# Kernel tuning notes

Measured on AMD Instinct MI355X. Metric: run time of the kernel, lower is better.

The kernel has to match this reference:

```python
import jax, jax.numpy as jnp
import numpy as np

H = 2048
NBINS = 256

def setup_inputs() -> dict:
    key = jax.random.key(0)
    k1, k2, k3, k4 = jax.random.split(key, 4)
    input_data = jax.random.uniform(k1, (1, 3, H, H), jnp.float32, -1.0, 1.0)
    target_data = jax.random.uniform(k2, (1, 3, H, H), jnp.float32, -1.0, 1.0)
    mask_src = (jax.random.uniform(k3, (1, 1, H, H)) > 0.5).astype(jnp.float32)
    mask_tar = (jax.random.uniform(k4, (1, 1, H, H)) > 0.5).astype(jnp.float32)
    return {"input_data": input_data, "target_data": target_data,
            "mask_src": mask_src, "mask_tar": mask_tar}


def _de_norm(x):
    # (x+1)/2 clamped to [0,1]
    return jnp.clip((x + 1.0) * 0.5, 0.0, 1.0)


def _masked_cdf(img, mask):
    # img: [3,H,W] in [0,255]; mask: [H,W] 0/1 weights.
    # Equivalent to np.histogram(masked_pixels, bins=256, range=(0,255)) per
    # channel followed by normalized cumsum: weighted bincount over all pixels.
    bins = jnp.clip(jnp.floor(img * (NBINS / 255.0)).astype(jnp.int32), 0, NBINS - 1)
    offs = bins + (jnp.arange(3, dtype=jnp.int32) * NBINS)[:, None, None]
    w = jnp.broadcast_to(mask, img.shape).reshape(-1)
    hist = jax.ops.segment_sum(w, offs.reshape(-1), num_segments=3 * NBINS)
    hist = hist.reshape(3, NBINS)
    cdf = jnp.cumsum(hist, axis=1)
    total = jnp.maximum(cdf[:, -1:], 1.0)  # number of masked pixels
    return cdf / total


def _cal_trans(dst_cdf, ref_cdf):
    # Faithful vectorization of PSGAN cal_trans: for i in 1..255, table[i] is
    # the first j in 1..255 with ref_cdf[j-1] <= dst_cdf[i] <= ref_cdf[j],
    # else i; table[0]=0, table[255]=255.
    j0 = jnp.searchsorted(ref_cdf, dst_cdf, side='left')
    cand = jnp.clip(j0, 1, NBINS - 1)
    ok = (ref_cdf[cand - 1] <= dst_cdf) & (ref_cdf[cand] >= dst_cdf)
    idx = jnp.arange(NBINS)
    table = jnp.where(ok, cand, idx)
    table = table.at[0].set(0).at[NBINS - 1].set(NBINS - 1)
    return table


def _histogram_loss(input_data, target_data, mask_src, mask_tar):
    inp = _de_norm(input_data)[0] * 255.0   # [3,H,W]
    tar = _de_norm(target_data)[0] * 255.0  # [3,H,W]
    ms = mask_src[0, 0]  # [H,W]
    mt = mask_tar[0, 0]
    input_masked = inp * ms
    target_masked = tar * mt

    cdf_dst = _masked_cdf(input_masked, ms)   # [3,256]
    cdf_ref = _masked_cdf(target_masked, mt)  # [3,256]
    tables = jax.vmap(_cal_trans)(cdf_dst, cdf_ref)  # [3,256] int

    # remap masked pixels through per-channel LUT (int() truncation)
    pix = jnp.clip(input_masked.astype(jnp.int32), 0, NBINS - 1)  # [3,H,W]
    matched = jnp.take_along_axis(tables, pix.reshape(3, -1), axis=1)
    matched = matched.reshape(input_masked.shape).astype(input_masked.dtype)
    input_match = jnp.where(ms[None] != 0, matched, input_masked)
    input_match = jax.lax.stop_gradient(input_match)  # to_var(requires_grad=False)

    return jnp.mean(jnp.abs(input_masked - input_match))


def reference(input_data, target_data, mask_src, mask_tar):
    return _histogram_loss(input_data, target_data, mask_src, mask_tar)
```

## Files before the change

kernel.cpp:

```cpp
#include <hip/hip_runtime.h>

#define HH 2048
#define NPIX (HH * HH)
#define NBINS 256
#define NQ (NPIX / 4)

#define GHIST_WORDS (6 * NBINS)
#define GPK_WORDS   (3 * NBINS)
#define WS_ZERO_BYTES (GHIST_WORDS * 4 + GPK_WORDS * 8)

#define FRAC_BITS 22
#define CNT_SHIFT 42
#define FRAC_MASK ((1ULL << CNT_SHIFT) - 1)

__device__ __forceinline__ float denorm255(float x) {
    return fminf(fmaxf((x + 1.0f) * 0.5f, 0.0f), 1.0f) * 255.0f;
}

__global__ __launch_bounds__(512, 8) void fused_hist(
        const float* __restrict__ in, const float* __restrict__ tar,
        const float* __restrict__ ms, const float* __restrict__ mt,
        unsigned* __restrict__ ghist, unsigned long long* __restrict__ gpk) {
    __shared__ unsigned lhs[3 * NBINS];
    __shared__ unsigned lht[3 * NBINS];
    __shared__ unsigned long long lpk[3 * NBINS];
    for (int i = threadIdx.x; i < 3 * NBINS; i += blockDim.x) {
        lhs[i] = 0u; lht[i] = 0u; lpk[i] = 0ull;
    }
    __syncthreads();

    const float BSCALE = 256.0f / 255.0f;
    const float FSCALE = 4194304.0f;
    const int stride = gridDim.x * blockDim.x;
    for (int idx = blockIdx.x * blockDim.x + threadIdx.x; idx < NQ; idx += stride) {
        float4 m4 = ((const float4*)ms)[idx];
        float4 t4 = ((const float4*)mt)[idx];
        float mv[4] = {m4.x, m4.y, m4.z, m4.w};
        float tv[4] = {t4.x, t4.y, t4.z, t4.w};
        #pragma unroll
        for (int ch = 0; ch < 3; ++ch) {
            float4 a = ((const float4*)(in  + (size_t)ch * NPIX))[idx];
            float4 b = ((const float4*)(tar + (size_t)ch * NPIX))[idx];
            float av[4] = {a.x, a.y, a.z, a.w};
            float bv[4] = {b.x, b.y, b.z, b.w};
            #pragma unroll
            for (int k = 0; k < 4; ++k) {
                if (mv[k] != 0.0f) {
                    float v = denorm255(av[k]);
                    int hb = min(max((int)floorf(v * BSCALE), 0), NBINS - 1);
                    atomicAdd(&lhs[ch * NBINS + hb], 1u);
                    int tb = min((int)v, NBINS - 1);
                    unsigned fr = (unsigned)((v - (float)tb) * FSCALE);
                    atomicAdd(&lpk[ch * NBINS + tb],
                              (1ULL << CNT_SHIFT) | (unsigned long long)fr);
                }
                if (tv[k] != 0.0f) {
                    float v = denorm255(bv[k]);
                    int hb = min(max((int)floorf(v * BSCALE), 0), NBINS - 1);
                    atomicAdd(&lht[ch * NBINS + hb], 1u);
                }
            }
        }
    }
    __syncthreads();
    for (int i = threadIdx.x; i < 3 * NBINS; i += blockDim.x) {
        unsigned a = lhs[i]; if (a) atomicAdd(&ghist[i], a);
        unsigned b = lht[i]; if (b) atomicAdd(&ghist[3 * NBINS + i], b);
        unsigned long long p = lpk[i]; if (p) atomicAdd(&gpk[i], p);
    }
}

__global__ __launch_bounds__(NBINS) void table_loss(
        const unsigned* __restrict__ ghist,
        const unsigned long long* __restrict__ gpk,
        float* __restrict__ out) {
    __shared__ float cdf[6][NBINS];
    __shared__ float tot[6];
    const int t = threadIdx.x;
    #pragma unroll
    for (int j = 0; j < 6; ++j) cdf[j][t] = (float)ghist[j * NBINS + t];
    __syncthreads();
    #pragma unroll
    for (int off = 1; off < NBINS; off <<= 1) {
        float add[6];
        #pragma unroll
        for (int j = 0; j < 6; ++j) add[j] = (t >= off) ? cdf[j][t - off] : 0.0f;
        __syncthreads();
        #pragma unroll
        for (int j = 0; j < 6; ++j) cdf[j][t] += add[j];
        __syncthreads();
    }
    if (t < 6) tot[t] = fmaxf(cdf[t][NBINS - 1], 1.0f);
    __syncthreads();
    #pragma unroll
    for (int j = 0; j < 6; ++j) cdf[j][t] = cdf[j][t] / tot[j];
    __syncthreads();

    double lsum = 0.0;
    #pragma unroll
    for (int ch = 0; ch < 3; ++ch) {
        const float d = cdf[ch][t];
        const float* ref = cdf[3 + ch];
        int lo = 0, hi = NBINS;
        while (lo < hi) {
            int mid = (lo + hi) >> 1;
            if (ref[mid] < d) lo = mid + 1; else hi = mid;
        }
        int cand = min(max(lo, 1), NBINS - 1);
        int T = (ref[cand - 1] <= d && ref[cand] >= d) ? cand : t;
        if (t == 0) T = 0;
        if (t == NBINS - 1) T = NBINS - 1;

        const int b = t;
        const unsigned long long pk = gpk[ch * NBINS + t];
        const double c = (double)(pk >> CNT_SHIFT);
        const double F = (double)(pk & FRAC_MASK) * (1.0 / 4194304.0);
        lsum += (T <= b) ? (c * (double)(b - T) + F)
                         : (c * (double)(T - b) - F);
    }
    #pragma unroll
    for (int off = 32; off; off >>= 1) lsum += __shfl_down(lsum, off, 64);
    __shared__ double wsum[4];
    if ((t & 63) == 0) wsum[t >> 6] = lsum;
    __syncthreads();
    if (t == 0)
        out[0] = (float)((wsum[0] + wsum[1] + wsum[2] + wsum[3]) / (double)(3 * NPIX));
}

extern "C" void kernel_launch(void* const* d_in, const int* in_sizes, int n_in,
                              void* d_out, int out_size, void* d_ws, size_t ws_size,
                              hipStream_t stream) {
    const float* in  = (const float*)d_in[0];
    const float* tar = (const float*)d_in[1];
    const float* ms  = (const float*)d_in[2];
    const float* mt  = (const float*)d_in[3];
    float* out = (float*)d_out;

    unsigned* ghist = (unsigned*)d_ws;
    unsigned long long* gpk = (unsigned long long*)((char*)d_ws + GHIST_WORDS * 4);

    hipMemsetAsync(d_ws, 0, WS_ZERO_BYTES, stream);
    fused_hist<<<1024, 512, 0, stream>>>(in, tar, ms, mt, ghist, gpk);
    table_loss<<<1, NBINS, 0, stream>>>(ghist, gpk, out);
}
```

Measured before the change: 166.4 us.

## Merge source histogram into packed 512-bin array and prefetch loads branchlessly

The separate source-histogram atomic is removed. Each masked source pixel now does one 64-bit atomic into a 512-entry per-channel array indexed by hb+tb, and the table kernel recovers both the 256-bin histogram and the truncation counts and fractions from even/odd pairs. The main loop gets a fixed trip count with register double-buffered prefetch of all eight float4 streams, and a grid of 512 blocks. Masking is branchless, adding zero instead of skipping, so atomics now run for unmasked pixels too, which trades divergence for extra LDS traffic.

```diff
diff --git a/kernel.cpp b/kernel.cpp
--- a/kernel.cpp
+++ b/kernel.cpp
@@ -3,82 +3,124 @@
 #define HH 2048
 #define NPIX (HH * HH)
 #define NBINS 256
+#define NRBINS 512
 #define NQ (NPIX / 4)
 
-#define GHIST_WORDS (6 * NBINS)
-#define GPK_WORDS   (3 * NBINS)
-#define WS_ZERO_BYTES (GHIST_WORDS * 4 + GPK_WORDS * 8)
+#define BLOCKS 512
+#define THREADS 512
+#define ITERS (NQ / (BLOCKS * THREADS))
 
-#define FRAC_BITS 22
 #define CNT_SHIFT 42
 #define FRAC_MASK ((1ULL << CNT_SHIFT) - 1)
+
+#define GPK_WORDS (3 * NRBINS)
+#define GHT_WORDS (3 * NBINS)
+#define WS_ZERO_BYTES (GPK_WORDS * 8 + GHT_WORDS * 4)
 
 __device__ __forceinline__ float denorm255(float x) {
     return fminf(fmaxf((x + 1.0f) * 0.5f, 0.0f), 1.0f) * 255.0f;
 }
 
-__global__ __launch_bounds__(512, 8) void fused_hist(
+__global__ __launch_bounds__(THREADS, 2) void fused_hist(
         const float* __restrict__ in, const float* __restrict__ tar,
         const float* __restrict__ ms, const float* __restrict__ mt,
-        unsigned* __restrict__ ghist, unsigned long long* __restrict__ gpk) {
-    __shared__ unsigned lhs[3 * NBINS];
+        unsigned long long* __restrict__ gpk, unsigned* __restrict__ ght) {
+    __shared__ unsigned long long lpk[3 * NRBINS];
     __shared__ unsigned lht[3 * NBINS];
-    __shared__ unsigned long long lpk[3 * NBINS];
-    for (int i = threadIdx.x; i < 3 * NBINS; i += blockDim.x) {
-        lhs[i] = 0u; lht[i] = 0u; lpk[i] = 0ull;
-    }
+    for (int i = threadIdx.x; i < 3 * NRBINS; i += THREADS) lpk[i] = 0ULL;
+    for (int i = threadIdx.x; i < 3 * NBINS; i += THREADS) lht[i] = 0u;
     __syncthreads();
 
     const float BSCALE = 256.0f / 255.0f;
     const float FSCALE = 4194304.0f;
-    const int stride = gridDim.x * blockDim.x;
-    for (int idx = blockIdx.x * blockDim.x + threadIdx.x; idx < NQ; idx += stride) {
-        float4 m4 = ((const float4*)ms)[idx];
-        float4 t4 = ((const float4*)mt)[idx];
-        float mv[4] = {m4.x, m4.y, m4.z, m4.w};
-        float tv[4] = {t4.x, t4.y, t4.z, t4.w};
+    const int stride = BLOCKS * THREADS;
+    int idx = blockIdx.x * THREADS + threadIdx.x;
+
+    float4 cm  = ((const float4*)ms)[idx];
+    float4 ct  = ((const float4*)mt)[idx];
+    float4 ca0 = ((const float4*)(in))[idx];
+    float4 ca1 = ((const float4*)(in + NPIX))[idx];
+    float4 ca2 = ((const float4*)(in + 2 * NPIX))[idx];
+    float4 cb0 = ((const float4*)(tar))[idx];
+    float4 cb1 = ((const float4*)(tar + NPIX))[idx];
+    float4 cb2 = ((const float4*)(tar + 2 * NPIX))[idx];
+
+    #pragma unroll
+    for (int s = 0; s < ITERS; ++s) {
+        float4 nm, nt4, na0, na1, na2, nb0, nb1, nb2;
+        const int nidx = idx + stride;
+        if (s < ITERS - 1) {
+            nm  = ((const float4*)ms)[nidx];
+            nt4 = ((const float4*)mt)[nidx];
+            na0 = ((const float4*)(in))[nidx];
+            na1 = ((const float4*)(in + NPIX))[nidx];
+            na2 = ((const float4*)(in + 2 * NPIX))[nidx];
+            nb0 = ((const float4*)(tar))[nidx];
+            nb1 = ((const float4*)(tar + NPIX))[nidx];
+            nb2 = ((const float4*)(tar + 2 * NPIX))[nidx];
+        }
+
+        const float mv[4] = {cm.x, cm.y, cm.z, cm.w};
+        const float tv[4] = {ct.x, ct.y, ct.z, ct.w};
+        const float av[3][4] = {{ca0.x, ca0.y, ca0.z, ca0.w},
+                                {ca1.x, ca1.y, ca1.z, ca1.w},
+                                {ca2.x, ca2.y, ca2.z, ca2.w}};
+        const float bv[3][4] = {{cb0.x, cb0.y, cb0.z, cb0.w},
+                                {cb1.x, cb1.y, cb1.z, cb1.w},
+                                {cb2.x, cb2.y, cb2.z, cb2.w}};
+
         #pragma unroll
         for (int ch = 0; ch < 3; ++ch) {
-            float4 a = ((const float4*)(in  + (size_t)ch * NPIX))[idx];
-            float4 b = ((const float4*)(tar + (size_t)ch * NPIX))[idx];
-            float av[4] = {a.x, a.y, a.z, a.w};
-            float bv[4] = {b.x, b.y, b.z, b.w};
             #pragma unroll
             for (int k = 0; k < 4; ++k) {
-                if (mv[k] != 0.0f) {
-                    float v = denorm255(av[k]);
-                    int hb = min(max((int)floorf(v * BSCALE), 0), NBINS - 1);
-                    atomicAdd(&lhs[ch * NBINS + hb], 1u);
-                    int tb = min((int)v, NBINS - 1);
-                    unsigned fr = (unsigned)((v - (float)tb) * FSCALE);
-                    atomicAdd(&lpk[ch * NBINS + tb],
-                              (1ULL << CNT_SHIFT) | (unsigned long long)fr);
-                }
-                if (tv[k] != 0.0f) {
-                    float v = denorm255(bv[k]);
-                    int hb = min(max((int)floorf(v * BSCALE), 0), NBINS - 1);
-                    atomicAdd(&lht[ch * NBINS + hb], 1u);
-                }
+                float v = denorm255(av[ch][k]);
+                int hb = min((int)(v * BSCALE), NBINS - 1);
+                int tb = (int)v;
+                unsigned fr = (unsigned)((v - (float)tb) * FSCALE);
+                unsigned long long pk =
+                    (1ULL << CNT_SHIFT) | (unsigned long long)fr;
+                pk = (mv[k] != 0.0f) ? pk : 0ULL;
+                atomicAdd(&lpk[ch * NRBINS + hb + tb], pk);
+
+                float w = denorm255(bv[ch][k]);
+                int wb = min((int)(w * BSCALE), NBINS - 1);
+                atomicAdd(&lht[ch * NBINS + wb], (tv[k] != 0.0f) ? 1u : 0u);
             }
         }
+        if (s < ITERS - 1) {
+            cm = nm; ct = nt4;
+            ca0 = na0; ca1 = na1; ca2 = na2;
+            cb0 = nb0; cb1 = nb1; cb2 = nb2;
+        }
+        idx = nidx;
     }
     __syncthreads();
-    for (int i = threadIdx.x; i < 3 * NBINS; i += blockDim.x) {
-        unsigned a = lhs[i]; if (a) atomicAdd(&ghist[i], a);
-        unsigned b = lht[i]; if (b) atomicAdd(&ghist[3 * NBINS + i], b);
-        unsigned long long p = lpk[i]; if (p) atomicAdd(&gpk[i], p);
+    for (int i = threadIdx.x; i < 3 * NRBINS; i += THREADS) {
+        unsigned long long p = lpk[i];
+        if (p) atomicAdd(&gpk[i], p);
+    }
+    for (int i = threadIdx.x; i < 3 * NBINS; i += THREADS) {
+        unsigned h = lht[i];
+        if (h) atomicAdd(&ght[i], h);
     }
 }
 
 __global__ __launch_bounds__(NBINS) void table_loss(
-        const unsigned* __restrict__ ghist,
         const unsigned long long* __restrict__ gpk,
-        float* __restrict__ out) {
+        const unsigned* __restrict__ ght, float* __restrict__ out) {
     __shared__ float cdf[6][NBINS];
     __shared__ float tot[6];
     const int t = threadIdx.x;
+
+    unsigned long long pe[3], po[3];
     #pragma unroll
-    for (int j = 0; j < 6; ++j) cdf[j][t] = (float)ghist[j * NBINS + t];
+    for (int ch = 0; ch < 3; ++ch) {
+        pe[ch] = gpk[ch * NRBINS + 2 * t];
+        po[ch] = gpk[ch * NRBINS + 2 * t + 1];
+        unsigned long long pp = (t > 0) ? gpk[ch * NRBINS + 2 * t - 1] : 0ULL;
+        cdf[ch][t] = (float)((pe[ch] >> CNT_SHIFT) + (pp >> CNT_SHIFT));
+        cdf[3 + ch][t] = (float)ght[ch * NBINS + t];
+    }
     __syncthreads();
     #pragma unroll
     for (int off = 1; off < NBINS; off <<= 1) {
@@ -112,9 +154,11 @@
         if (t == NBINS - 1) T = NBINS - 1;
 
         const int b = t;
-        const unsigned long long pk = gpk[ch * NBINS + t];
-        const double c = (double)(pk >> CNT_SHIFT);
-        const double F = (double)(pk & FRAC_MASK) * (1.0 / 4194304.0);
+        const double c =
+            (double)((pe[ch] >> CNT_SHIFT) + (po[ch] >> CNT_SHIFT));
+        const double F =
+            (double)((pe[ch] & FRAC_MASK) + (po[ch] & FRAC_MASK)) *
+            (1.0 / 4194304.0);
         lsum += (T <= b) ? (c * (double)(b - T) + F)
                          : (c * (double)(T - b) - F);
     }
@@ -124,7 +168,8 @@
     if ((t & 63) == 0) wsum[t >> 6] = lsum;
     __syncthreads();
     if (t == 0)
-        out[0] = (float)((wsum[0] + wsum[1] + wsum[2] + wsum[3]) / (double)(3 * NPIX));
+        out[0] = (float)((wsum[0] + wsum[1] + wsum[2] + wsum[3]) /
+                         (double)(3 * NPIX));
 }
 
 extern "C" void kernel_launch(void* const* d_in, const int* in_sizes, int n_in,
@@ -136,10 +181,10 @@
     const float* mt  = (const float*)d_in[3];
     float* out = (float*)d_out;
 
-    unsigned* ghist = (unsigned*)d_ws;
-    unsigned long long* gpk = (unsigned long long*)((char*)d_ws + GHIST_WORDS * 4);
+    unsigned long long* gpk = (unsigned long long*)d_ws;
+    unsigned* ght = (unsigned*)((char*)d_ws + GPK_WORDS * 8);
 
     hipMemsetAsync(d_ws, 0, WS_ZERO_BYTES, stream);
-    fused_hist<<<1024, 512, 0, stream>>>(in, tar, ms, mt, ghist, gpk);
-    table_loss<<<1, NBINS, 0, stream>>>(ghist, gpk, out);
+    fused_hist<<<BLOCKS, THREADS, 0, stream>>>(in, tar, ms, mt, gpk, ght);
+    table_loss<<<1, NBINS, 0, stream>>>(gpk, ght, out);
 }
```

Measured after the change: 160.7 us. 1.04x faster.
